# Performance work log

Hardware: AMD Instinct MI355X
Metric: run time of the kernel (lower is better)

Reference implementation:

```python
import jax, jax.numpy as jnp
import numpy as np

N_NODES = 65536
IN_CH = 512
HIDDEN = 256          # hidden_channels[0] == encoder_hidden
OUT_CH = 8
NUM_GRAPHS = 32
MAX_LEN = 4096        # static pad bound (>= max per-graph length)
BN_EPS = 1e-5


def _make_batch_ids():
    # deterministic ragged per-graph lengths summing exactly to N_NODES
    rng = np.random.RandomState(0)
    d = rng.randint(-512, 512, size=NUM_GRAPHS)
    d[-1] -= d.sum()
    lengths = N_NODES // NUM_GRAPHS + d          # each in ~[1536, 2560] <= MAX_LEN
    return jnp.asarray(np.repeat(np.arange(NUM_GRAPHS), lengths), dtype=jnp.int32)


def setup_inputs() -> dict:
    key = jax.random.key(0)
    ks = jax.random.split(key, 12)
    f32 = jnp.float32
    inp = {
        'x_res': jax.random.normal(ks[0], (N_NODES, IN_CH), dtype=f32),
        'batch': _make_batch_ids(),
        # BatchNorm1d affine params
        'bn_gamma': jnp.ones((IN_CH,), f32),
        'bn_beta': jnp.zeros((IN_CH,), f32),
        # input2transformer: Linear(C,2H) GELU Linear(2H,H) GELU Linear(H,H)
        'W1': jax.random.normal(ks[1], (IN_CH, 2 * HIDDEN), f32) * (1.0 / np.sqrt(IN_CH)),
        'b1': jnp.zeros((2 * HIDDEN,), f32),
        'W2': jax.random.normal(ks[2], (2 * HIDDEN, HIDDEN), f32) * (1.0 / np.sqrt(2 * HIDDEN)),
        'b2': jnp.zeros((HIDDEN,), f32),
        'W3': jax.random.normal(ks[3], (HIDDEN, HIDDEN), f32) * (1.0 / np.sqrt(HIDDEN)),
        'b3': jnp.zeros((HIDDEN,), f32),
        # out_angles: Linear(encoder_hidden, out_ch) GELU DynamicTanh Tanh
        'Wo': jax.random.normal(ks[4], (HIDDEN, OUT_CH), f32) * (1.0 / np.sqrt(HIDDEN)),
        'bo': jnp.zeros((OUT_CH,), f32),
        'dyt_alpha': jnp.asarray(0.5, f32),
        'dyt_w': jnp.ones((OUT_CH,), f32),
        'dyt_b': jnp.zeros((OUT_CH,), f32),
    }
    return inp


def _forward(x_res, batch, bn_gamma, bn_beta, W1, b1, W2, b2, W3, b3,
             Wo, bo, dyt_alpha, dyt_w, dyt_b):
    # BatchNorm1d (training-mode batch stats, biased var), dropout is identity (eval)
    mu = jnp.mean(x_res, axis=0)
    var = jnp.mean((x_res - mu) ** 2, axis=0)
    x = (x_res - mu) * jax.lax.rsqrt(var + BN_EPS) * bn_gamma + bn_beta
    # input2transformer MLP (torch GELU default = exact erf)
    gelu = lambda t: jax.nn.gelu(t, approximate=False)
    x = gelu(x @ W1 + b1)
    x = gelu(x @ W2 + b2)
    x = x @ W3 + b3                                   # [N, HIDDEN]
    # ragged -> padded: scatter each node into (graph, position-in-graph)
    counts = jax.ops.segment_sum(jnp.ones_like(batch, dtype=jnp.int32), batch,
                                 num_segments=NUM_GRAPHS)
    offsets = jnp.concatenate([jnp.zeros((1,), jnp.int32),
                               jnp.cumsum(counts)[:-1].astype(jnp.int32)])
    pos = jnp.arange(N_NODES, dtype=jnp.int32) - offsets[batch]
    x_pad = jnp.zeros((NUM_GRAPHS, MAX_LEN, HIDDEN), x.dtype).at[batch, pos].set(x)
    z = jnp.transpose(x_pad, (1, 0, 2))               # [MAX_LEN, NUM_GRAPHS, HIDDEN] (stack dim=1)
    # out_angles head: Linear -> GELU -> DynamicTanh -> Tanh
    a = gelu(z @ Wo + bo)
    a = dyt_w * jnp.tanh(dyt_alpha * a) + dyt_b       # DynamicTanh (channels_last)
    return jnp.tanh(a)                                # [MAX_LEN, NUM_GRAPHS, OUT_CH]


def reference(x_res, batch, bn_gamma, bn_beta, W1, b1, W2, b2, W3, b3,
              Wo, bo, dyt_alpha, dyt_w, dyt_b):
    return _forward(x_res, batch, bn_gamma, bn_beta, W1, b1, W2, b2, W3, b3,
                    Wo, bo, dyt_alpha, dyt_w, dyt_b)
```

## Files before the change

### kernel.cpp

```cpp
#include <hip/hip_runtime.h>
#include <hip/hip_bf16.h>

#define N_NODES 65536
#define IN_CH 512
#define HIDDEN 256
#define OUT_CH 8
#define NUM_GRAPHS 32
#define MAX_LEN 4096
#define BN_EPS 1e-5f
#define BN_BLOCKS 2048

using short8  = __attribute__((ext_vector_type(8))) short;
using floatx4 = __attribute__((ext_vector_type(4))) float;
typedef unsigned int u32;
typedef unsigned short u16;

__device__ inline u16 f2b(float f) {
    u32 u = __float_as_uint(f);
    u += 0x7FFFu + ((u >> 16) & 1u);
    return (u16)(u >> 16);
}
__device__ inline float gelu_f(float x) {
    float z = x + 0.044715f * x * x * x;
    float e = __builtin_exp2f(-2.3022078f * z);
    return x * __builtin_amdgcn_rcpf(1.0f + e);
}
__device__ inline float tanh_f(float y) {
    y = fminf(fmaxf(y, -20.0f), 20.0f);
    float t = __builtin_exp2f(2.885390082f * y);
    return (t - 1.0f) * __builtin_amdgcn_rcpf(t + 1.0f);
}
__device__ inline void load_lds16(const void* g, void* l) {
    __builtin_amdgcn_global_load_lds(
        (const __attribute__((address_space(1))) u32*)g,
        (__attribute__((address_space(3))) u32*)l, 16, 0, 0);
}

__global__ __launch_bounds__(256) void statscast_k(const float* __restrict__ x,
                                                   u16* __restrict__ xb,
                                                   float4* __restrict__ partials) {
    __shared__ float4 sS[128];
    __shared__ float4 sQ[128];
    int tid = threadIdx.x;
    int half = tid >> 7;
    int c = tid & 127;
    const float4* x4 = (const float4*)x;
    uint2* xb2 = (uint2*)xb;
    float4 s = make_float4(0.f, 0.f, 0.f, 0.f);
    float4 q = make_float4(0.f, 0.f, 0.f, 0.f);
    int row0 = blockIdx.x * 32;
#pragma unroll
    for (int r = half; r < 32; r += 2) {
        size_t off = (size_t)(row0 + r) * 128 + c;
        float4 v = x4[off];
        s.x += v.x; s.y += v.y; s.z += v.z; s.w += v.w;
        q.x += v.x * v.x; q.y += v.y * v.y; q.z += v.z * v.z; q.w += v.w * v.w;
        uint2 o;
        o.x = (u32)f2b(v.x) | ((u32)f2b(v.y) << 16);
        o.y = (u32)f2b(v.z) | ((u32)f2b(v.w) << 16);
        xb2[off] = o;
    }
    if (half == 1) { sS[c] = s; sQ[c] = q; }
    __syncthreads();
    if (half == 0) {
        float4 s2 = sS[c], q2 = sQ[c];
        s.x += s2.x; s.y += s2.y; s.z += s2.z; s.w += s2.w;
        q.x += q2.x; q.y += q2.y; q.z += q2.z; q.w += q2.w;
        partials[(size_t)blockIdx.x * 256 + c * 2]     = make_float4(s.x, q.x, s.y, q.y);
        partials[(size_t)blockIdx.x * 256 + c * 2 + 1] = make_float4(s.z, q.z, s.w, q.w);
    }
}

__global__ __launch_bounds__(256) void bn_reduce_k(const float4* __restrict__ partials,
                                                   const float* __restrict__ gamma,
                                                   const float* __restrict__ beta,
                                                   float* __restrict__ scale,
                                                   float* __restrict__ shift) {
    __shared__ float4 sd[256];
    int tid = threadIdx.x;
    int g = blockIdx.x;
    float4 a = make_float4(0.f, 0.f, 0.f, 0.f);
    for (int r = tid; r < BN_BLOCKS; r += 256) {
        float4 v = partials[(size_t)r * 256 + g];
        a.x += v.x; a.y += v.y; a.z += v.z; a.w += v.w;
    }
    sd[tid] = a;
    __syncthreads();
    for (int st = 128; st > 0; st >>= 1) {
        if (tid < st) {
            float4 b = sd[tid + st];
            float4 m = sd[tid];
            m.x += b.x; m.y += b.y; m.z += b.z; m.w += b.w;
            sd[tid] = m;
        }
        __syncthreads();
    }
    if (tid == 0) {
        float4 t = sd[0];
        int c0 = g * 2, c1 = g * 2 + 1;
        const float inv = 1.0f / N_NODES;
        float mu0 = t.x * inv, var0 = t.y * inv - mu0 * mu0;
        float mu1 = t.z * inv, var1 = t.w * inv - mu1 * mu1;
        float sc0 = gamma[c0] * rsqrtf(var0 + BN_EPS);
        float sc1 = gamma[c1] * rsqrtf(var1 + BN_EPS);
        scale[c0] = sc0; shift[c0] = beta[c0] - mu0 * sc0;
        scale[c1] = sc1; shift[c1] = beta[c1] - mu1 * sc1;
    }
}

__global__ __launch_bounds__(256) void prep_k(const float* __restrict__ W1,
                                              const float* __restrict__ W2,
                                              const float* __restrict__ W3,
                                              const float* __restrict__ b1,
                                              const float* __restrict__ scale,
                                              const float* __restrict__ shift,
                                              u16* __restrict__ W1T,
                                              u16* __restrict__ W2T,
                                              u16* __restrict__ W3T,
                                              float* __restrict__ b1f,
                                              const int* __restrict__ batch,
                                              int* __restrict__ offsets) {
    int bid = blockIdx.x;
    int tid = threadIdx.x;
    if (bid < 1792) {
        int idx = bid * 256 + tid;
        if (idx < 262144) {
            int k = idx >> 9, m = idx & 511;
            W1T[(size_t)m * 512 + k] = f2b(scale[k] * W1[idx]);
        } else if (idx < 262144 + 131072) {
            int i = idx - 262144;
            int k = i >> 8, m = i & 255;
            W2T[(size_t)m * 512 + k] = f2b(W2[i]);
        } else {
            int i = idx - 393216;
            int k = i >> 8, m = i & 255;
            W3T[(size_t)m * 256 + k] = f2b(W3[i]);
        }
        if (bid == 0 && tid < NUM_GRAPHS + 1) {
            int gph = tid;
            int lo = 0, hi = N_NODES;
            while (lo < hi) {
                int mid = (lo + hi) >> 1;
                if (batch[mid] < gph) lo = mid + 1; else hi = mid;
            }
            offsets[gph] = lo;
        }
    } else {
        int m = (bid - 1792) * 256 + tid;
        float acc = b1[m];
#pragma unroll 16
        for (int k = 0; k < 512; ++k) acc += shift[k] * W1[k * 512 + m];
        b1f[m] = acc;
    }
}

template <int DO_GELU, int NXB>
__global__ __launch_bounds__(512) void gemm_bt_k(const u16* __restrict__ A,
                                                 const u16* __restrict__ BT,
                                                 const float* __restrict__ bias,
                                                 u16* __restrict__ C,
                                                 int K, int M) {
    __shared__ __align__(16) u16 As[256 * 64];
    __shared__ __align__(16) u16 Bs[128 * 64];
    int tid = threadIdx.x;
    int lane = tid & 63;
    int bid = blockIdx.x;
    int xcd = bid & 7;
    int slot = bid >> 3;
    int rloc = slot / NXB;
    int colb = slot - rloc * NXB;
    int row0 = (xcd * 32 + rloc) * 256;
    int col0 = colb * 128;
    int wave = tid >> 6;
    int wr = (wave >> 1) * 64;
    int wc = (wave & 1) * 64;
    int l15 = lane & 15;
    int q = lane >> 4;

    floatx4 acc[4][4] = {};

    const int nkt = K >> 6;
    for (int kt = 0; kt < nkt; ++kt) {
        int k0 = kt << 6;
#pragma unroll
        for (int s = 0; s < 4; ++s) {
            int li = s * 512 + tid;
            int r = li >> 3;
            int g = li & 7;
            int gs = g ^ (r & 7);
            load_lds16(&A[(size_t)(row0 + r) * K + k0 + gs * 8], &As[li * 8]);
        }
#pragma unroll
        for (int s = 0; s < 2; ++s) {
            int li = s * 512 + tid;
            int r = li >> 3;
            int g = li & 7;
            int gs = g ^ (r & 7);
            load_lds16(&BT[(size_t)(col0 + r) * K + k0 + gs * 8], &Bs[li * 8]);
        }
        __syncthreads();
#pragma unroll
        for (int ks = 0; ks < 2; ++ks) {
            int gidx = ks * 4 + q;
            short8 af[4], bg[4];
#pragma unroll
            for (int i = 0; i < 4; ++i) {
                int row = wr + i * 16 + l15;
                af[i] = *(const short8*)&As[row * 64 + (gidx ^ (row & 7)) * 8];
            }
#pragma unroll
            for (int j = 0; j < 4; ++j) {
                int row = wc + j * 16 + l15;
                bg[j] = *(const short8*)&Bs[row * 64 + (gidx ^ (row & 7)) * 8];
            }
#pragma unroll
            for (int i = 0; i < 4; ++i)
#pragma unroll
                for (int j = 0; j < 4; ++j)
                    acc[i][j] = __builtin_amdgcn_mfma_f32_16x16x32_bf16(bg[j], af[i], acc[i][j], 0, 0, 0);
        }
        __syncthreads();
    }
#pragma unroll
    for (int i = 0; i < 4; ++i) {
        size_t rbase = (size_t)(row0 + wr + i * 16 + l15) * M;
#pragma unroll
        for (int j = 0; j < 4; ++j) {
            int c = col0 + wc + j * 16 + q * 4;
            float4 b4 = *(const float4*)&bias[c];
            float v0 = acc[i][j][0] + b4.x;
            float v1 = acc[i][j][1] + b4.y;
            float v2 = acc[i][j][2] + b4.z;
            float v3 = acc[i][j][3] + b4.w;
            if (DO_GELU) { v0 = gelu_f(v0); v1 = gelu_f(v1); v2 = gelu_f(v2); v3 = gelu_f(v3); }
            uint2 pk;
            pk.x = (u32)f2b(v0) | ((u32)f2b(v1) << 16);
            pk.y = (u32)f2b(v2) | ((u32)f2b(v3) << 16);
            *(uint2*)&C[rbase + c] = pk;
        }
    }
}

__global__ __launch_bounds__(256) void head_k(const u16* __restrict__ h3,
                                              const float* __restrict__ Wo,
                                              const float* __restrict__ bo,
                                              const int* __restrict__ offsets,
                                              const float* __restrict__ alpha_p,
                                              const float* __restrict__ dyt_w,
                                              const float* __restrict__ dyt_b,
                                              float* __restrict__ out) {
    __shared__ float sWo[HIDDEN * OUT_CH];
    __shared__ int soff[NUM_GRAPHS + 1];
    int tid = threadIdx.x;
#pragma unroll
    for (int i = 0; i < 8; ++i) sWo[i * 256 + tid] = Wo[i * 256 + tid];
    if (tid < NUM_GRAPHS + 1) soff[tid] = offsets[tid];
    __syncthreads();
    int idx = blockIdx.x * 256 + tid;
    int g = idx & 31;
    int p = idx >> 5;
    int n = soff[g] + p;
    bool valid = n < soff[g + 1];
    float acc[8];
#pragma unroll
    for (int c = 0; c < 8; ++c) acc[c] = bo[c];
    if (valid) {
        const uint4* hr = (const uint4*)(h3 + (size_t)n * HIDDEN);
#pragma unroll 4
        for (int kk = 0; kk < 32; ++kk) {
            uint4 v = hr[kk];
            u32 u[4] = {v.x, v.y, v.z, v.w};
#pragma unroll
            for (int pp = 0; pp < 4; ++pp) {
                float h0 = __uint_as_float(u[pp] << 16);
                float h1 = __uint_as_float(u[pp] & 0xFFFF0000u);
                const float* w0 = &sWo[(kk * 8 + pp * 2) * 8];
                const float* w1 = w0 + 8;
#pragma unroll
                for (int c = 0; c < 8; ++c) acc[c] += h0 * w0[c];
#pragma unroll
                for (int c = 0; c < 8; ++c) acc[c] += h1 * w1[c];
            }
        }
    }
    float alpha = alpha_p[0];
    float res[8];
#pragma unroll
    for (int c = 0; c < 8; ++c) {
        float a = gelu_f(acc[c]);
        a = dyt_w[c] * tanh_f(alpha * a) + dyt_b[c];
        res[c] = tanh_f(a);
    }
    float4* o = (float4*)(out + (size_t)idx * OUT_CH);
    o[0] = make_float4(res[0], res[1], res[2], res[3]);
    o[1] = make_float4(res[4], res[5], res[6], res[7]);
}

extern "C" void kernel_launch(void* const* d_in, const int* in_sizes, int n_in,
                              void* d_out, int out_size, void* d_ws, size_t ws_size,
                              hipStream_t stream) {
    (void)in_sizes; (void)n_in; (void)out_size; (void)ws_size;
    const float* x_res = (const float*)d_in[0];
    const int*   batch = (const int*)d_in[1];
    const float* gamma = (const float*)d_in[2];
    const float* beta  = (const float*)d_in[3];
    const float* W1    = (const float*)d_in[4];
    const float* b1    = (const float*)d_in[5];
    const float* W2    = (const float*)d_in[6];
    const float* b2    = (const float*)d_in[7];
    const float* W3    = (const float*)d_in[8];
    const float* b3    = (const float*)d_in[9];
    const float* Wo    = (const float*)d_in[10];
    const float* bo    = (const float*)d_in[11];
    const float* alpha = (const float*)d_in[12];
    const float* dyt_w = (const float*)d_in[13];
    const float* dyt_b = (const float*)d_in[14];
    float* out = (float*)d_out;

    char* ws = (char*)d_ws;
    float* scale = (float*)(ws + 0);
    float* shift = (float*)(ws + 2048);
    float* b1f   = (float*)(ws + 4096);
    int*   offs  = (int*)(ws + 8192);
    u16* W1T = (u16*)(ws + 16384);
    u16* W2T = (u16*)(ws + 16384 + 524288);
    u16* W3T = (u16*)(ws + 16384 + 524288 + 262144);
    const size_t MB = 1024 * 1024;
    u16* xb = (u16*)(ws + 2 * MB);
    u16* h1 = (u16*)(ws + 66 * MB);
    u16* h2 = (u16*)(ws + 2 * MB);
    u16* h3 = (u16*)(ws + 66 * MB);
    float4* partials = (float4*)(ws + 66 * MB);

    statscast_k<<<BN_BLOCKS, 256, 0, stream>>>(x_res, xb, partials);
    bn_reduce_k<<<256, 256, 0, stream>>>(partials, gamma, beta, scale, shift);
    prep_k<<<1794, 256, 0, stream>>>(W1, W2, W3, b1, scale, shift,
                                     W1T, W2T, W3T, b1f, batch, offs);
    gemm_bt_k<1, 4><<<1024, 512, 0, stream>>>(xb, W1T, b1f, h1, 512, 512);
    gemm_bt_k<1, 2><<<512, 512, 0, stream>>>(h1, W2T, b2, h2, 512, 256);
    gemm_bt_k<0, 2><<<512, 512, 0, stream>>>(h2, W3T, b3, h3, 256, 256);
    head_k<<<512, 256, 0, stream>>>(h3, Wo, bo, offs, alpha, dyt_w, dyt_b, out);
}
```

Before: 383.2 us.

## Double-buffer LDS in GEMM with 256x256 tiles and interleaved load/MFMA schedule

```diff
diff --git a/kernel.cpp b/kernel.cpp
--- a/kernel.cpp
+++ b/kernel.cpp
@@ -154,14 +154,16 @@
     }
 }
 
+#define FENCE asm volatile("" ::: "memory")
+
 template <int DO_GELU, int NXB>
-__global__ __launch_bounds__(512) void gemm_bt_k(const u16* __restrict__ A,
-                                                 const u16* __restrict__ BT,
-                                                 const float* __restrict__ bias,
-                                                 u16* __restrict__ C,
-                                                 int K, int M) {
-    __shared__ __align__(16) u16 As[256 * 64];
-    __shared__ __align__(16) u16 Bs[128 * 64];
+__global__ __launch_bounds__(512, 2) void gemm_bt8_k(const u16* __restrict__ A,
+                                                     const u16* __restrict__ BT,
+                                                     const float* __restrict__ bias,
+                                                     u16* __restrict__ C,
+                                                     int K, int M) {
+    __shared__ __align__(16) u16 As[2][256 * 64];
+    __shared__ __align__(16) u16 Bs[2][256 * 64];
     int tid = threadIdx.x;
     int lane = tid & 63;
     int bid = blockIdx.x;
@@ -170,59 +172,107 @@
     int rloc = slot / NXB;
     int colb = slot - rloc * NXB;
     int row0 = (xcd * 32 + rloc) * 256;
-    int col0 = colb * 128;
+    int col0 = colb * 256;
     int wave = tid >> 6;
-    int wr = (wave >> 1) * 64;
-    int wc = (wave & 1) * 64;
+    int wr = (wave >> 2) * 128;
+    int wc = (wave & 3) * 64;
     int l15 = lane & 15;
     int q = lane >> 4;
 
-    floatx4 acc[4][4] = {};
-
-    const int nkt = K >> 6;
-    for (int kt = 0; kt < nkt; ++kt) {
-        int k0 = kt << 6;
-#pragma unroll
-        for (int s = 0; s < 4; ++s) {
-            int li = s * 512 + tid;
-            int r = li >> 3;
-            int g = li & 7;
-            int gs = g ^ (r & 7);
-            load_lds16(&A[(size_t)(row0 + r) * K + k0 + gs * 8], &As[li * 8]);
-        }
-#pragma unroll
-        for (int s = 0; s < 2; ++s) {
-            int li = s * 512 + tid;
-            int r = li >> 3;
-            int g = li & 7;
-            int gs = g ^ (r & 7);
-            load_lds16(&BT[(size_t)(col0 + r) * K + k0 + gs * 8], &Bs[li * 8]);
-        }
-        __syncthreads();
-#pragma unroll
-        for (int ks = 0; ks < 2; ++ks) {
-            int gidx = ks * 4 + q;
-            short8 af[4], bg[4];
-#pragma unroll
-            for (int i = 0; i < 4; ++i) {
-                int row = wr + i * 16 + l15;
-                af[i] = *(const short8*)&As[row * 64 + (gidx ^ (row & 7)) * 8];
-            }
-#pragma unroll
-            for (int j = 0; j < 4; ++j) {
-                int row = wc + j * 16 + l15;
-                bg[j] = *(const short8*)&Bs[row * 64 + (gidx ^ (row & 7)) * 8];
-            }
-#pragma unroll
-            for (int i = 0; i < 4; ++i)
-#pragma unroll
-                for (int j = 0; j < 4; ++j)
-                    acc[i][j] = __builtin_amdgcn_mfma_f32_16x16x32_bf16(bg[j], af[i], acc[i][j], 0, 0, 0);
-        }
-        __syncthreads();
-    }
-#pragma unroll
-    for (int i = 0; i < 4; ++i) {
+    floatx4 acc[8][4] = {};
+
+    const u16* pA[4];
+    const u16* pB[4];
+    int ldst[4];
+#pragma unroll
+    for (int s = 0; s < 4; ++s) {
+        int li = s * 512 + tid;
+        int r = li >> 3;
+        int g = li & 7;
+        int gs = g ^ (r & 7);
+        pA[s] = A + (size_t)(row0 + r) * K + gs * 8;
+        pB[s] = BT + (size_t)(col0 + r) * K + gs * 8;
+        ldst[s] = li * 8;
+    }
+
+#define LOAD_AF(BASE, GIDX)                                                    \
+    _Pragma("unroll")                                                          \
+    for (int i = 0; i < 4; ++i) {                                              \
+        int row = (BASE) + i * 16 + l15;                                       \
+        af[i] = *(const short8*)&As[cur][row * 64 + ((GIDX) ^ (row & 7)) * 8]; \
+    }
+#define LOAD_BG(BASE, GIDX)                                                    \
+    _Pragma("unroll")                                                          \
+    for (int j = 0; j < 4; ++j) {                                              \
+        int row = (BASE) + j * 16 + l15;                                       \
+        bg[j] = *(const short8*)&Bs[cur][row * 64 + ((GIDX) ^ (row & 7)) * 8]; \
+    }
+#define MFMA16(IB)                                                             \
+    __builtin_amdgcn_s_setprio(1);                                             \
+    _Pragma("unroll")                                                          \
+    for (int i = 0; i < 4; ++i)                                                \
+        _Pragma("unroll")                                                      \
+        for (int j = 0; j < 4; ++j)                                            \
+            acc[(IB) + i][j] = __builtin_amdgcn_mfma_f32_16x16x32_bf16(        \
+                bg[j], af[i], acc[(IB) + i][j], 0, 0, 0);                      \
+    __builtin_amdgcn_s_setprio(0)
+
+#pragma unroll
+    for (int s = 0; s < 4; ++s) load_lds16(pA[s], &As[0][ldst[s]]);
+#pragma unroll
+    for (int s = 0; s < 4; ++s) load_lds16(pB[s], &Bs[0][ldst[s]]);
+
+    const int nt = K >> 6;
+    for (int t = 0; t < nt; ++t) {
+        const int cur = t & 1;
+        const int nx = cur ^ 1;
+        const int kn = (t + 1 < nt) ? ((t + 1) << 6) : 0;
+        short8 af[4], bg[4];
+
+        load_lds16(pA[0] + kn, &As[nx][ldst[0]]);
+        load_lds16(pA[1] + kn, &As[nx][ldst[1]]);
+        asm volatile("s_waitcnt vmcnt(2)" ::: "memory");
+        __builtin_amdgcn_s_barrier();
+        FENCE;
+        LOAD_AF(wr, q);
+        LOAD_BG(wc, q);
+        MFMA16(0);
+        FENCE;
+        __builtin_amdgcn_s_barrier();
+        LOAD_AF(wr + 64, q);
+        load_lds16(pA[2] + kn, &As[nx][ldst[2]]);
+        load_lds16(pA[3] + kn, &As[nx][ldst[3]]);
+        FENCE;
+        __builtin_amdgcn_s_barrier();
+        FENCE;
+        MFMA16(4);
+        FENCE;
+        __builtin_amdgcn_s_barrier();
+        LOAD_AF(wr, 4 + q);
+        LOAD_BG(wc, 4 + q);
+        load_lds16(pB[0] + kn, &Bs[nx][ldst[0]]);
+        load_lds16(pB[1] + kn, &Bs[nx][ldst[1]]);
+        FENCE;
+        __builtin_amdgcn_s_barrier();
+        FENCE;
+        MFMA16(0);
+        FENCE;
+        __builtin_amdgcn_s_barrier();
+        LOAD_AF(wr + 64, 4 + q);
+        load_lds16(pB[2] + kn, &Bs[nx][ldst[2]]);
+        load_lds16(pB[3] + kn, &Bs[nx][ldst[3]]);
+        FENCE;
+        __builtin_amdgcn_s_barrier();
+        FENCE;
+        MFMA16(4);
+        FENCE;
+        __builtin_amdgcn_s_barrier();
+        FENCE;
+    }
+    asm volatile("s_waitcnt vmcnt(0)" ::: "memory");
+
+#pragma unroll
+    for (int i = 0; i < 8; ++i) {
         size_t rbase = (size_t)(row0 + wr + i * 16 + l15) * M;
 #pragma unroll
         for (int j = 0; j < 4; ++j) {
@@ -239,6 +289,9 @@
             *(uint2*)&C[rbase + c] = pk;
         }
     }
+#undef LOAD_AF
+#undef LOAD_BG
+#undef MFMA16
 }
 
 __global__ __launch_bounds__(256) void head_k(const u16* __restrict__ h3,
@@ -336,8 +389,8 @@
     bn_reduce_k<<<256, 256, 0, stream>>>(partials, gamma, beta, scale, shift);
     prep_k<<<1794, 256, 0, stream>>>(W1, W2, W3, b1, scale, shift,
                                      W1T, W2T, W3T, b1f, batch, offs);
-    gemm_bt_k<1, 4><<<1024, 512, 0, stream>>>(xb, W1T, b1f, h1, 512, 512);
-    gemm_bt_k<1, 2><<<512, 512, 0, stream>>>(h1, W2T, b2, h2, 512, 256);
-    gemm_bt_k<0, 2><<<512, 512, 0, stream>>>(h2, W3T, b3, h3, 256, 256);
+    gemm_bt8_k<1, 2><<<512, 512, 0, stream>>>(xb, W1T, b1f, h1, 512, 512);
+    gemm_bt8_k<1, 1><<<256, 512, 0, stream>>>(h1, W2T, b2, h2, 512, 256);
+    gemm_bt8_k<0, 1><<<256, 512, 0, stream>>>(h2, W3T, b3, h3, 256, 256);
     head_k<<<512, 256, 0, stream>>>(h3, Wo, bo, offs, alpha, dyt_w, dyt_b, out);
 }
```

New measurement: 392.2 us. 1.02x slower.

## Fuse second and third MLP GEMMs into one kernel keeping h2 in LDS

Applied to the files above, without the earlier changes.

```diff
diff --git a/kernel.cpp b/kernel.cpp
--- a/kernel.cpp
+++ b/kernel.cpp
@@ -241,6 +241,202 @@
     }
 }
 
+#define FENCE asm volatile("" ::: "memory")
+
+__global__ __launch_bounds__(512, 2) void gemm23_k(const u16* __restrict__ A,
+                                                   const u16* __restrict__ B2T,
+                                                   const float* __restrict__ b2v,
+                                                   const u16* __restrict__ W3T,
+                                                   const float* __restrict__ b3v,
+                                                   u16* __restrict__ C) {
+    __shared__ __align__(16) u16 lds[65536];
+    int tid = threadIdx.x;
+    int lane = tid & 63;
+    int bid = blockIdx.x;
+    int xcd = bid & 7;
+    int slot = bid >> 3;
+    int row0 = (xcd * 32 + slot) * 256;
+    int wave = tid >> 6;
+    int wr = (wave >> 2) * 128;
+    int wc = (wave & 3) * 64;
+    int l15 = lane & 15;
+    int q = lane >> 4;
+
+    floatx4 acc[8][4] = {};
+
+    const u16* pA[4];
+    const u16* pB[4];
+    int ldst[4];
+#pragma unroll
+    for (int s = 0; s < 4; ++s) {
+        int li = s * 512 + tid;
+        int r = li >> 3;
+        int g = li & 7;
+        int gs = g ^ (r & 7);
+        pA[s] = A + (size_t)(row0 + r) * 512 + gs * 8;
+        pB[s] = B2T + (size_t)r * 512 + gs * 8;
+        ldst[s] = li * 8;
+    }
+
+#define LDA2(BASE, GIDX)                                                             \
+    _Pragma("unroll")                                                                \
+    for (int i = 0; i < 4; ++i) {                                                    \
+        int row = (BASE) + i * 16 + l15;                                             \
+        af[i] = *(const short8*)&lds[curA + row * 64 + (((GIDX) ^ (row & 7)) << 3)]; \
+    }
+#define LDB2(BASE, GIDX)                                                             \
+    _Pragma("unroll")                                                                \
+    for (int j = 0; j < 4; ++j) {                                                    \
+        int row = (BASE) + j * 16 + l15;                                             \
+        bg[j] = *(const short8*)&lds[curB + row * 64 + (((GIDX) ^ (row & 7)) << 3)]; \
+    }
+#define MFMA16(IB)                                                                   \
+    __builtin_amdgcn_s_setprio(1);                                                   \
+    _Pragma("unroll")                                                                \
+    for (int i = 0; i < 4; ++i)                                                      \
+        _Pragma("unroll")                                                            \
+        for (int j = 0; j < 4; ++j)                                                  \
+            acc[(IB) + i][j] = __builtin_amdgcn_mfma_f32_16x16x32_bf16(              \
+                bg[j], af[i], acc[(IB) + i][j], 0, 0, 0);                            \
+    __builtin_amdgcn_s_setprio(0)
+
+#pragma unroll
+    for (int s = 0; s < 4; ++s) load_lds16(pA[s], &lds[ldst[s]]);
+#pragma unroll
+    for (int s = 0; s < 4; ++s) load_lds16(pB[s], &lds[32768 + ldst[s]]);
+
+    const int nt = 8;
+    for (int t = 0; t < nt; ++t) {
+        const int cur = t & 1;
+        const int nx = cur ^ 1;
+        const bool last = (t + 1 == nt);
+        const int kn = (t + 1) << 6;
+        const int curA = cur * 16384, curB = 32768 + cur * 16384;
+        const int nxA = nx * 16384,  nxB = 32768 + nx * 16384;
+        short8 af[4], bg[4];
+
+        if (!last) {
+            load_lds16(pA[0] + kn, &lds[nxA + ldst[0]]);
+            load_lds16(pA[1] + kn, &lds[nxA + ldst[1]]);
+        }
+        if (last) asm volatile("s_waitcnt vmcnt(0)" ::: "memory");
+        else      asm volatile("s_waitcnt vmcnt(2)" ::: "memory");
+        __builtin_amdgcn_s_barrier();
+        FENCE;
+        LDA2(wr, q);
+        LDB2(wc, q);
+        MFMA16(0);
+        FENCE;
+        __builtin_amdgcn_s_barrier();
+        LDA2(wr + 64, q);
+        if (!last) {
+            load_lds16(pA[2] + kn, &lds[nxA + ldst[2]]);
+            load_lds16(pA[3] + kn, &lds[nxA + ldst[3]]);
+        }
+        FENCE;
+        __builtin_amdgcn_s_barrier();
+        FENCE;
+        MFMA16(4);
+        FENCE;
+        __builtin_amdgcn_s_barrier();
+        LDA2(wr, 4 + q);
+        LDB2(wc, 4 + q);
+        if (!last) {
+            load_lds16(pB[0] + kn, &lds[nxB + ldst[0]]);
+            load_lds16(pB[1] + kn, &lds[nxB + ldst[1]]);
+        }
+        FENCE;
+        __builtin_amdgcn_s_barrier();
+        FENCE;
+        MFMA16(0);
+        FENCE;
+        __builtin_amdgcn_s_barrier();
+        LDA2(wr + 64, 4 + q);
+        if (!last) {
+            load_lds16(pB[2] + kn, &lds[nxB + ldst[2]]);
+            load_lds16(pB[3] + kn, &lds[nxB + ldst[3]]);
+        }
+        FENCE;
+        __builtin_amdgcn_s_barrier();
+        FENCE;
+        MFMA16(4);
+        FENCE;
+        __builtin_amdgcn_s_barrier();
+        FENCE;
+    }
+    __syncthreads();
+
+#pragma unroll
+    for (int i = 0; i < 8; ++i) {
+        int row = wr + i * 16 + l15;
+#pragma unroll
+        for (int j = 0; j < 4; ++j) {
+            int c = wc + j * 16 + q * 4;
+            float4 b4 = *(const float4*)&b2v[c];
+            float v0 = gelu_f(acc[i][j][0] + b4.x);
+            float v1 = gelu_f(acc[i][j][1] + b4.y);
+            float v2 = gelu_f(acc[i][j][2] + b4.z);
+            float v3 = gelu_f(acc[i][j][3] + b4.w);
+            uint2 pk;
+            pk.x = (u32)f2b(v0) | ((u32)f2b(v1) << 16);
+            pk.y = (u32)f2b(v2) | ((u32)f2b(v3) << 16);
+            int gr = c >> 3;
+            int addr = row * 256 + ((gr ^ (row & 7)) << 3) + (q & 1) * 4;
+            *(uint2*)&lds[addr] = pk;
+        }
+    }
+    __syncthreads();
+
+#pragma unroll
+    for (int i = 0; i < 8; ++i)
+#pragma unroll
+        for (int j = 0; j < 4; ++j)
+            acc[i][j] = (floatx4){0.f, 0.f, 0.f, 0.f};
+
+    for (int ks = 0; ks < 8; ++ks) {
+        int gidx = ks * 4 + q;
+        short8 af[8], bg[4];
+#pragma unroll
+        for (int j = 0; j < 4; ++j) {
+            int colr = wc + j * 16 + l15;
+            bg[j] = *(const short8*)&W3T[(size_t)colr * 256 + gidx * 8];
+        }
+#pragma unroll
+        for (int i = 0; i < 8; ++i) {
+            int row = wr + i * 16 + l15;
+            af[i] = *(const short8*)&lds[row * 256 + ((gidx ^ (row & 7)) << 3)];
+        }
+        __builtin_amdgcn_s_setprio(1);
+#pragma unroll
+        for (int i = 0; i < 8; ++i)
+#pragma unroll
+            for (int j = 0; j < 4; ++j)
+                acc[i][j] = __builtin_amdgcn_mfma_f32_16x16x32_bf16(bg[j], af[i], acc[i][j], 0, 0, 0);
+        __builtin_amdgcn_s_setprio(0);
+    }
+
+#pragma unroll
+    for (int i = 0; i < 8; ++i) {
+        size_t rbase = (size_t)(row0 + wr + i * 16 + l15) * 256;
+#pragma unroll
+        for (int j = 0; j < 4; ++j) {
+            int c = wc + j * 16 + q * 4;
+            float4 b4 = *(const float4*)&b3v[c];
+            float v0 = acc[i][j][0] + b4.x;
+            float v1 = acc[i][j][1] + b4.y;
+            float v2 = acc[i][j][2] + b4.z;
+            float v3 = acc[i][j][3] + b4.w;
+            uint2 pk;
+            pk.x = (u32)f2b(v0) | ((u32)f2b(v1) << 16);
+            pk.y = (u32)f2b(v2) | ((u32)f2b(v3) << 16);
+            *(uint2*)&C[rbase + c] = pk;
+        }
+    }
+#undef LDA2
+#undef LDB2
+#undef MFMA16
+}
+
 __global__ __launch_bounds__(256) void head_k(const u16* __restrict__ h3,
                                               const float* __restrict__ Wo,
                                               const float* __restrict__ bo,
@@ -328,8 +524,7 @@
     const size_t MB = 1024 * 1024;
     u16* xb = (u16*)(ws + 2 * MB);
     u16* h1 = (u16*)(ws + 66 * MB);
-    u16* h2 = (u16*)(ws + 2 * MB);
-    u16* h3 = (u16*)(ws + 66 * MB);
+    u16* h3 = (u16*)(ws + 2 * MB);
     float4* partials = (float4*)(ws + 66 * MB);
 
     statscast_k<<<BN_BLOCKS, 256, 0, stream>>>(x_res, xb, partials);
@@ -337,7 +532,6 @@
     prep_k<<<1794, 256, 0, stream>>>(W1, W2, W3, b1, scale, shift,
                                      W1T, W2T, W3T, b1f, batch, offs);
     gemm_bt_k<1, 4><<<1024, 512, 0, stream>>>(xb, W1T, b1f, h1, 512, 512);
-    gemm_bt_k<1, 2><<<512, 512, 0, stream>>>(h1, W2T, b2, h2, 512, 256);
-    gemm_bt_k<0, 2><<<512, 512, 0, stream>>>(h2, W3T, b3, h3, 256, 256);
+    gemm23_k<<<256, 512, 0, stream>>>(h1, W2T, b2, W3T, b3, h3);
     head_k<<<512, 256, 0, stream>>>(h3, Wo, bo, offs, alpha, dyt_w, dyt_b, out);
 }
```

New measurement: 374.3 us. 2.3% less time.
